# Kernel optimization log

Measured on AMD Instinct MI355X. Metric: run time of the kernel, lower is better.

## Reference

```python
import jax, jax.numpy as jnp
import numpy as np

EPS = 1e-4  # clamp floor used by RecFunction
B, C, D = 8192, 62, 8


def _rec(M):
    # Rectify SPD matrix: clamp eigenvalues at EPS. For SPD input, torch.svd's
    # (U, S) coincide with the eigendecomposition, so eigh is the faithful
    # (and efficient, symmetry-exploiting) batched equivalent.
    w, U = jnp.linalg.eigh(M)                      # w: [B,D], U: [B,D,D]
    return (U * jnp.maximum(w, EPS)[..., None, :]) @ jnp.swapaxes(U, -1, -2)


def _logm(M):
    # Matrix log via eigendecomposition (eigenvalues >= EPS after _rec).
    w, U = jnp.linalg.eigh(M)
    return (U * jnp.log(w)[..., None, :]) @ jnp.swapaxes(U, -1, -2)


def setup_inputs() -> dict:
    key = jax.random.key(0)
    kx, k1, k2, k3 = jax.random.split(key, 4)
    A = jax.random.normal(kx, (B, C, C), dtype=jnp.float32)
    X = (A @ jnp.swapaxes(A, 1, 2)) / C            # SPD covariance-like input [B,62,62]
    w1 = jax.random.normal(k1, (C, D), dtype=jnp.float32)
    w2 = jax.random.normal(k2, (D, D), dtype=jnp.float32)
    fc = jax.random.normal(k3, (D * D, 2), dtype=jnp.float32)
    return {"X": X, "w1": w1, "w2": w2, "fc": fc}


def reference(X, w1, w2, fc):
    # BiMap 62->8, rectify
    out = _rec(jnp.einsum('ca,bcd,de->bae', w1, X, w1))   # [B,8,8]
    # BiMap 8->8, rectify
    out = _rec(jnp.einsum('ca,bcd,de->bae', w2, out, w2)) # [B,8,8]
    # LogEig
    out = _logm(out)                                      # [B,8,8]
    feat = out.reshape(out.shape[0], -1)                  # [B,64]
    logits = feat @ fc                                    # [B,2]
    return jax.nn.log_softmax(logits, axis=1), feat
```

## Files before the change

kernel.cpp:

```cpp
#include <hip/hip_runtime.h>
#include <math.h>

#define B_TOTAL 8192
#define C_DIM 62
#define CC (C_DIM * C_DIM)
#define EPSV 1e-4f
#define NSWEEP 4
#define WSTRIDE 72
#define YSTR 9


template<int M> __device__ __forceinline__ float sx(float x) {
  int xi = __builtin_bit_cast(int, x);
  int r;
  if constexpr (M == 1)      r = __builtin_amdgcn_update_dpp(xi, xi, 0xB1, 0xF, 0xF, false);
  else if constexpr (M == 2) r = __builtin_amdgcn_update_dpp(xi, xi, 0x4E, 0xF, 0xF, false);
  else if constexpr (M == 3) r = __builtin_amdgcn_update_dpp(xi, xi, 0x1B, 0xF, 0xF, false);
  else                       r = __builtin_amdgcn_ds_swizzle(xi, (M << 10) | 0x1F);
  return __builtin_bit_cast(float, r);
}

__device__ __forceinline__ void xperm8(float r[8], const int e) {
  const bool b0 = (e & 1) != 0, b1 = (e & 2) != 0, b2 = (e & 4) != 0;
  float t0[8], t1[8];
#pragma unroll
  for (int j = 0; j < 8; ++j) t0[j] = b0 ? r[j ^ 1] : r[j];
#pragma unroll
  for (int j = 0; j < 8; ++j) t1[j] = b1 ? t0[j ^ 2] : t0[j];
#pragma unroll
  for (int j = 0; j < 8; ++j) r[j] = b2 ? t1[j ^ 4] : t1[j];
}

template<int M>
__device__ __forceinline__ void jstage(float ar[8], float pr[8], const int e) {
  constexpr int HB = (M >= 4) ? 4 : ((M >= 2) ? 2 : 1);
  constexpr int A1 = (M == 1) ? 2 : 1;
  constexpr int A2 = (M <= 3) ? 4 : 2;
  const bool low = (e & HB) == 0;
  float d_oth = sx<M>(ar[0]);
  float o_oth = sx<M>(ar[M]);
  float apq = 0.5f * (ar[M] + o_oth);
  float app = low ? ar[0] : d_oth;
  float aqq = low ? d_oth : ar[0];
  float taun = aqq - app;
  float den = fabsf(taun) + sqrtf(fmaf(taun, taun, 4.f * apq * apq)) + 1e-38f;
  float t = (2.f * apq) * copysignf(1.f, taun) * __builtin_amdgcn_rcpf(den);
  float c = rsqrtf(fmaf(t, t, 1.f));
  float s = t * c;
  float cg[8], sg[8];
  cg[0] = c;  sg[0] = s;
  cg[A1] = sx<A1>(c);  sg[A1] = sx<A1>(s);
  cg[A2] = sx<A2>(c);  sg[A2] = sx<A2>(s);
  cg[A1 ^ A2] = sx<A2>(cg[A1]);  sg[A1 ^ A2] = sx<A2>(sg[A1]);
  float an[8], pn[8];
#pragma unroll
  for (int d = 0; d < 8; ++d) {
    constexpr int T0 = 0;
    const int rep = (d == T0 || d == A1 || d == A2 || d == (A1 ^ A2)) ? d : (d ^ M);
    const bool flip = (d & HB) != 0;
    float sD = sg[rep];
    float ss = (low != flip) ? -sD : sD;
    an[d] = fmaf(cg[rep], ar[d], ss * ar[d ^ M]);
    pn[d] = fmaf(cg[rep], pr[d], ss * pr[d ^ M]);
  }
#pragma unroll
  for (int d = 0; d < 8; ++d) pr[d] = pn[d];
  float scol = low ? -s : s;
  float aoth[8];
#pragma unroll
  for (int d = 0; d < 8; ++d) aoth[d] = sx<M>(an[d ^ M]);
#pragma unroll
  for (int d = 0; d < 8; ++d) ar[d] = fmaf(c, an[d], scol * aoth[d]);
}

__device__ __forceinline__ void jacobi8rel(float ar[8], float u[8], const int e) {
  float pr[8];
#pragma unroll
  for (int i = 0; i < 8; ++i) pr[i] = (i == 0) ? 1.f : 0.f;
#pragma unroll 1
  for (int sweep = 0; sweep < NSWEEP; ++sweep) {
    jstage<1>(ar, pr, e);
    jstage<2>(ar, pr, e);
    jstage<3>(ar, pr, e);
    jstage<4>(ar, pr, e);
    jstage<5>(ar, pr, e);
    jstage<6>(ar, pr, e);
    jstage<7>(ar, pr, e);
  }
  u[0] = pr[0];
  u[1] = sx<1>(pr[1]);
  u[2] = sx<2>(pr[2]);
  u[3] = sx<3>(pr[3]);
  u[4] = sx<4>(pr[4]);
  u[5] = sx<5>(pr[5]);
  u[6] = sx<6>(pr[6]);
  u[7] = sx<7>(pr[7]);
  xperm8(u, e);
}

__global__ __launch_bounds__(64) void spdnet_kernel(
    const float* __restrict__ X, const float* __restrict__ w1,
    const float* __restrict__ w2, const float* __restrict__ fc,
    float* __restrict__ out) {
  __shared__ __align__(16) float w1s[C_DIM * 8];
  __shared__ float Ys[C_DIM * YSTR];
  __shared__ float M1s[8 * 64];
  __shared__ __align__(16) float Wbuf[8 * WSTRIDE];
  __shared__ float lwbuf[64];
  __shared__ float w2s[64];
  __shared__ float fcs[128];
  const int lane = threadIdx.x;
  const int b0 = blockIdx.x * 8;

  w2s[lane] = w2[lane];
  fcs[lane] = fc[lane];
  fcs[lane + 64] = fc[lane + 64];
  if (lane < C_DIM) {
    *(float4*)(w1s + lane * 8)     = *(const float4*)(w1 + lane * 8);
    *(float4*)(w1s + lane * 8 + 4) = *(const float4*)(w1 + lane * 8 + 4);
  }

  float xrA[C_DIM], xrB[C_DIM];
  if (lane < C_DIM) {
    const float* row = X + (size_t)b0 * CC + lane * C_DIM;
#pragma unroll
    for (int k = 0; k < 31; ++k) {
      float2 t = *(const float2*)(row + 2 * k);
      xrA[2 * k] = t.x; xrA[2 * k + 1] = t.y;
    }
  }
  __syncthreads();

  auto loadrow = [&](float* r, int g) {
    if (lane < C_DIM) {
      const float* row = X + (size_t)(b0 + g) * CC + lane * C_DIM;
#pragma unroll
      for (int k = 0; k < 31; ++k) {
        float2 t = *(const float2*)(row + 2 * k);
        r[2 * k] = t.x; r[2 * k + 1] = t.y;
      }
    }
  };
  auto computeA = [&](const float* xr, int g) {
    if (lane < C_DIM) {
      float a0=0.f,a1=0.f,a2=0.f,a3=0.f,a4=0.f,a5=0.f,a6=0.f,a7=0.f;
#pragma unroll
      for (int d = 0; d < C_DIM; ++d) {
        float x = xr[d];
        const float* wr = w1 + d * 8;
        a0 = fmaf(x, wr[0], a0); a1 = fmaf(x, wr[1], a1);
        a2 = fmaf(x, wr[2], a2); a3 = fmaf(x, wr[3], a3);
        a4 = fmaf(x, wr[4], a4); a5 = fmaf(x, wr[5], a5);
        a6 = fmaf(x, wr[6], a6); a7 = fmaf(x, wr[7], a7);
      }
      float* yr = Ys + lane * YSTR;
      yr[0]=a0; yr[1]=a1; yr[2]=a2; yr[3]=a3;
      yr[4]=a4; yr[5]=a5; yr[6]=a6; yr[7]=a7;
    }
    __syncthreads();
    {
      const int a_ = lane >> 3, e_ = lane & 7;
      float s = 0.f;
#pragma unroll
      for (int c = 0; c < C_DIM; ++c)
        s = fmaf(w1s[c * 8 + a_], Ys[c * YSTR + e_], s);
      M1s[g * 64 + lane] = s;
    }
    __syncthreads();
  };

#pragma unroll 1
  for (int g = 0; g < 8; g += 2) {
    loadrow(xrB, g + 1);
    computeA(xrA, g);
    if (g + 2 < 8) loadrow(xrA, g + 2);
    computeA(xrB, g + 1);
  }

  const int e = lane & 7;
  const int g = lane >> 3;
  float a[8], u[8], m2[8];
  float* Wg = &Wbuf[g * WSTRIDE];

#pragma unroll
  for (int j = 0; j < 8; ++j) a[j] = M1s[g * 64 + e * 8 + j];

  {
    float t[8];
#pragma unroll
    for (int j = 0; j < 8; ++j) t[j] = 0.f;
#pragma unroll
    for (int k = 0; k < 8; ++k) {
      float4 q0 = *(const float4*)(w2s + k * 8);
      float4 q1 = *(const float4*)(w2s + k * 8 + 4);
      t[0] = fmaf(a[k], q0.x, t[0]); t[1] = fmaf(a[k], q0.y, t[1]);
      t[2] = fmaf(a[k], q0.z, t[2]); t[3] = fmaf(a[k], q0.w, t[3]);
      t[4] = fmaf(a[k], q1.x, t[4]); t[5] = fmaf(a[k], q1.y, t[5]);
      t[6] = fmaf(a[k], q1.z, t[6]); t[7] = fmaf(a[k], q1.w, t[7]);
    }
#pragma unroll
    for (int j = 0; j < 8; ++j) Wg[e * 8 + j] = t[j];
  }
  __syncthreads();
  {
    float tcol[8];
#pragma unroll
    for (int k = 0; k < 8; ++k) tcol[k] = Wg[k * 8 + e];
#pragma unroll
    for (int i = 0; i < 8; ++i) m2[i] = 0.f;
#pragma unroll
    for (int k = 0; k < 8; ++k) {
      float4 q0 = *(const float4*)(w2s + k * 8);
      float4 q1 = *(const float4*)(w2s + k * 8 + 4);
      m2[0] = fmaf(q0.x, tcol[k], m2[0]); m2[1] = fmaf(q0.y, tcol[k], m2[1]);
      m2[2] = fmaf(q0.z, tcol[k], m2[2]); m2[3] = fmaf(q0.w, tcol[k], m2[3]);
      m2[4] = fmaf(q1.x, tcol[k], m2[4]); m2[5] = fmaf(q1.y, tcol[k], m2[5]);
      m2[6] = fmaf(q1.z, tcol[k], m2[6]); m2[7] = fmaf(q1.w, tcol[k], m2[7]);
    }
  }
  __syncthreads();

  xperm8(m2, e);
  jacobi8rel(m2, u, e);
  float lw = logf(fmaxf(m2[0], EPSV));
#pragma unroll
  for (int i = 0; i < 8; ++i) Wg[e * 8 + i] = u[i];
  lwbuf[g * 8 + e] = lw;
  __syncthreads();
  {
    float mk[8];
#pragma unroll
    for (int k = 0; k < 8; ++k) mk[k] = lwbuf[g * 8 + k] * Wg[k * 8 + e];
    float fcol[8];
#pragma unroll
    for (int i = 0; i < 8; ++i) fcol[i] = 0.f;
#pragma unroll
    for (int k = 0; k < 8; ++k) {
      float4 q0 = *(const float4*)&Wg[k * 8 + 0];
      float4 q1 = *(const float4*)&Wg[k * 8 + 4];
      fcol[0] = fmaf(q0.x, mk[k], fcol[0]); fcol[1] = fmaf(q0.y, mk[k], fcol[1]);
      fcol[2] = fmaf(q0.z, mk[k], fcol[2]); fcol[3] = fmaf(q0.w, mk[k], fcol[3]);
      fcol[4] = fmaf(q1.x, mk[k], fcol[4]); fcol[5] = fmaf(q1.y, mk[k], fcol[5]);
      fcol[6] = fmaf(q1.z, mk[k], fcol[6]); fcol[7] = fmaf(q1.w, mk[k], fcol[7]);
    }
    float l0 = 0.f, l1 = 0.f;
    const int b = b0 + g;
    float* featg = out + 2 * (size_t)B_TOTAL + (size_t)b * 64;
#pragma unroll
    for (int i = 0; i < 8; ++i) {
      featg[i * 8 + e] = fcol[i];
      l0 = fmaf(fcol[i], fcs[(i * 8 + e) * 2 + 0], l0);
      l1 = fmaf(fcol[i], fcs[(i * 8 + e) * 2 + 1], l1);
    }
    l0 += sx<1>(l0); l0 += sx<2>(l0); l0 += sx<4>(l0);
    l1 += sx<1>(l1); l1 += sx<2>(l1); l1 += sx<4>(l1);
    float mx = fmaxf(l0, l1);
    float lse = mx + logf(expf(l0 - mx) + expf(l1 - mx));
    if (e < 2) out[(size_t)b * 2 + e] = (e ? l1 : l0) - lse;
  }
}

extern "C" void kernel_launch(void* const* d_in, const int* in_sizes, int n_in,
                              void* d_out, int out_size, void* d_ws, size_t ws_size,
                              hipStream_t stream) {
  const float* X  = (const float*)d_in[0];
  const float* w1 = (const float*)d_in[1];
  const float* w2 = (const float*)d_in[2];
  const float* fc = (const float*)d_in[3];
  float* out = (float*)d_out;

  spdnet_kernel<<<B_TOTAL / 8, 64, 0, stream>>>(X, w1, w2, fc, out);
}
```

Measured before the change: 37.69 us.

## Process 16 batches per block with two waves, interleave two Jacobi solves in one wave

Blocks now handle 16 matrices with 128 threads: both wavefronts load and project their own 8 X matrices through the 62->8 BiMap. After that, only wave 0 runs the second BiMap, the Jacobi eigensolver and the LogEig/FC tail, interleaving two independent 8x8 solves per lane to expose instruction-level parallelism. This halves the grid and amortizes weight loads, but wave 1 idles through the serial Jacobi phase, and register pressure grows from holding two matrices per lane.

```diff
diff --git a/kernel.cpp b/kernel.cpp
--- a/kernel.cpp
+++ b/kernel.cpp
@@ -6,9 +6,9 @@
 #define CC (C_DIM * C_DIM)
 #define EPSV 1e-4f
 #define NSWEEP 4
+#define NBB 16
 #define WSTRIDE 72
 #define YSTR 9
-
 
 template<int M> __device__ __forceinline__ float sx(float x) {
   int xi = __builtin_bit_cast(int, x);
@@ -32,97 +32,118 @@
 }
 
 template<int M>
-__device__ __forceinline__ void jstage(float ar[8], float pr[8], const int e) {
+__device__ __forceinline__ void jstage2(float ar1[8], float pr1[8],
+                                        float ar2[8], float pr2[8], const int e) {
   constexpr int HB = (M >= 4) ? 4 : ((M >= 2) ? 2 : 1);
   constexpr int A1 = (M == 1) ? 2 : 1;
   constexpr int A2 = (M <= 3) ? 4 : 2;
   const bool low = (e & HB) == 0;
-  float d_oth = sx<M>(ar[0]);
-  float o_oth = sx<M>(ar[M]);
-  float apq = 0.5f * (ar[M] + o_oth);
-  float app = low ? ar[0] : d_oth;
-  float aqq = low ? d_oth : ar[0];
-  float taun = aqq - app;
-  float den = fabsf(taun) + sqrtf(fmaf(taun, taun, 4.f * apq * apq)) + 1e-38f;
-  float t = (2.f * apq) * copysignf(1.f, taun) * __builtin_amdgcn_rcpf(den);
-  float c = rsqrtf(fmaf(t, t, 1.f));
-  float s = t * c;
-  float cg[8], sg[8];
-  cg[0] = c;  sg[0] = s;
-  cg[A1] = sx<A1>(c);  sg[A1] = sx<A1>(s);
-  cg[A2] = sx<A2>(c);  sg[A2] = sx<A2>(s);
-  cg[A1 ^ A2] = sx<A2>(cg[A1]);  sg[A1 ^ A2] = sx<A2>(sg[A1]);
-  float an[8], pn[8];
+  float d1 = sx<M>(ar1[0]);
+  float d2 = sx<M>(ar2[0]);
+  float o1 = sx<M>(ar1[M]);
+  float o2 = sx<M>(ar2[M]);
+  float apq1 = 0.5f * (ar1[M] + o1);
+  float apq2 = 0.5f * (ar2[M] + o2);
+  float app1 = low ? ar1[0] : d1, aqq1 = low ? d1 : ar1[0];
+  float app2 = low ? ar2[0] : d2, aqq2 = low ? d2 : ar2[0];
+  float tn1 = aqq1 - app1;
+  float tn2 = aqq2 - app2;
+  float den1 = fabsf(tn1) + sqrtf(fmaf(tn1, tn1, 4.f * apq1 * apq1)) + 1e-38f;
+  float den2 = fabsf(tn2) + sqrtf(fmaf(tn2, tn2, 4.f * apq2 * apq2)) + 1e-38f;
+  float t1 = (2.f * apq1) * copysignf(1.f, tn1) * __builtin_amdgcn_rcpf(den1);
+  float t2 = (2.f * apq2) * copysignf(1.f, tn2) * __builtin_amdgcn_rcpf(den2);
+  float c1 = rsqrtf(fmaf(t1, t1, 1.f));
+  float c2 = rsqrtf(fmaf(t2, t2, 1.f));
+  float s1 = t1 * c1;
+  float s2 = t2 * c2;
+  float cg1[8], sg1[8], cg2[8], sg2[8];
+  cg1[0] = c1; sg1[0] = s1; cg2[0] = c2; sg2[0] = s2;
+  cg1[A1] = sx<A1>(c1); cg2[A1] = sx<A1>(c2);
+  sg1[A1] = sx<A1>(s1); sg2[A1] = sx<A1>(s2);
+  cg1[A2] = sx<A2>(c1); cg2[A2] = sx<A2>(c2);
+  sg1[A2] = sx<A2>(s1); sg2[A2] = sx<A2>(s2);
+  cg1[A1 ^ A2] = sx<A2>(cg1[A1]); cg2[A1 ^ A2] = sx<A2>(cg2[A1]);
+  sg1[A1 ^ A2] = sx<A2>(sg1[A1]); sg2[A1 ^ A2] = sx<A2>(sg2[A1]);
+  float an1[8], pn1[8], an2[8], pn2[8];
 #pragma unroll
   for (int d = 0; d < 8; ++d) {
-    constexpr int T0 = 0;
-    const int rep = (d == T0 || d == A1 || d == A2 || d == (A1 ^ A2)) ? d : (d ^ M);
+    const int rep = (d == 0 || d == A1 || d == A2 || d == (A1 ^ A2)) ? d : (d ^ M);
     const bool flip = (d & HB) != 0;
-    float sD = sg[rep];
-    float ss = (low != flip) ? -sD : sD;
-    an[d] = fmaf(cg[rep], ar[d], ss * ar[d ^ M]);
-    pn[d] = fmaf(cg[rep], pr[d], ss * pr[d ^ M]);
-  }
-#pragma unroll
-  for (int d = 0; d < 8; ++d) pr[d] = pn[d];
-  float scol = low ? -s : s;
-  float aoth[8];
-#pragma unroll
-  for (int d = 0; d < 8; ++d) aoth[d] = sx<M>(an[d ^ M]);
-#pragma unroll
-  for (int d = 0; d < 8; ++d) ar[d] = fmaf(c, an[d], scol * aoth[d]);
-}
-
-__device__ __forceinline__ void jacobi8rel(float ar[8], float u[8], const int e) {
-  float pr[8];
-#pragma unroll
-  for (int i = 0; i < 8; ++i) pr[i] = (i == 0) ? 1.f : 0.f;
+    float ss1 = (low != flip) ? -sg1[rep] : sg1[rep];
+    float ss2 = (low != flip) ? -sg2[rep] : sg2[rep];
+    an1[d] = fmaf(cg1[rep], ar1[d], ss1 * ar1[d ^ M]);
+    an2[d] = fmaf(cg2[rep], ar2[d], ss2 * ar2[d ^ M]);
+    pn1[d] = fmaf(cg1[rep], pr1[d], ss1 * pr1[d ^ M]);
+    pn2[d] = fmaf(cg2[rep], pr2[d], ss2 * pr2[d ^ M]);
+  }
+#pragma unroll
+  for (int d = 0; d < 8; ++d) { pr1[d] = pn1[d]; pr2[d] = pn2[d]; }
+  float sc1 = low ? -s1 : s1;
+  float sc2 = low ? -s2 : s2;
+  float ao1[8], ao2[8];
+#pragma unroll
+  for (int d = 0; d < 8; ++d) { ao1[d] = sx<M>(an1[d ^ M]); ao2[d] = sx<M>(an2[d ^ M]); }
+#pragma unroll
+  for (int d = 0; d < 8; ++d) {
+    ar1[d] = fmaf(c1, an1[d], sc1 * ao1[d]);
+    ar2[d] = fmaf(c2, an2[d], sc2 * ao2[d]);
+  }
+}
+
+__device__ __forceinline__ void jacobi8rel2(float ar1[8], float u1[8],
+                                            float ar2[8], float u2[8], const int e) {
+  float pr1[8], pr2[8];
+#pragma unroll
+  for (int i = 0; i < 8; ++i) { pr1[i] = (i == 0) ? 1.f : 0.f; pr2[i] = pr1[i]; }
 #pragma unroll 1
   for (int sweep = 0; sweep < NSWEEP; ++sweep) {
-    jstage<1>(ar, pr, e);
-    jstage<2>(ar, pr, e);
-    jstage<3>(ar, pr, e);
-    jstage<4>(ar, pr, e);
-    jstage<5>(ar, pr, e);
-    jstage<6>(ar, pr, e);
-    jstage<7>(ar, pr, e);
-  }
-  u[0] = pr[0];
-  u[1] = sx<1>(pr[1]);
-  u[2] = sx<2>(pr[2]);
-  u[3] = sx<3>(pr[3]);
-  u[4] = sx<4>(pr[4]);
-  u[5] = sx<5>(pr[5]);
-  u[6] = sx<6>(pr[6]);
-  u[7] = sx<7>(pr[7]);
-  xperm8(u, e);
-}
-
-__global__ __launch_bounds__(64) void spdnet_kernel(
+    jstage2<1>(ar1, pr1, ar2, pr2, e);
+    jstage2<2>(ar1, pr1, ar2, pr2, e);
+    jstage2<3>(ar1, pr1, ar2, pr2, e);
+    jstage2<4>(ar1, pr1, ar2, pr2, e);
+    jstage2<5>(ar1, pr1, ar2, pr2, e);
+    jstage2<6>(ar1, pr1, ar2, pr2, e);
+    jstage2<7>(ar1, pr1, ar2, pr2, e);
+  }
+  u1[0] = pr1[0];                u2[0] = pr2[0];
+  u1[1] = sx<1>(pr1[1]);         u2[1] = sx<1>(pr2[1]);
+  u1[2] = sx<2>(pr1[2]);         u2[2] = sx<2>(pr2[2]);
+  u1[3] = sx<3>(pr1[3]);         u2[3] = sx<3>(pr2[3]);
+  u1[4] = sx<4>(pr1[4]);         u2[4] = sx<4>(pr2[4]);
+  u1[5] = sx<5>(pr1[5]);         u2[5] = sx<5>(pr2[5]);
+  u1[6] = sx<6>(pr1[6]);         u2[6] = sx<6>(pr2[6]);
+  u1[7] = sx<7>(pr1[7]);         u2[7] = sx<7>(pr2[7]);
+  xperm8(u1, e);
+  xperm8(u2, e);
+}
+
+__global__ __launch_bounds__(128) void spdnet_kernel(
     const float* __restrict__ X, const float* __restrict__ w1,
     const float* __restrict__ w2, const float* __restrict__ fc,
     float* __restrict__ out) {
   __shared__ __align__(16) float w1s[C_DIM * 8];
-  __shared__ float Ys[C_DIM * YSTR];
-  __shared__ float M1s[8 * 64];
-  __shared__ __align__(16) float Wbuf[8 * WSTRIDE];
-  __shared__ float lwbuf[64];
+  __shared__ float Ys[2][C_DIM * YSTR];
+  __shared__ float M1s[NBB * 64];
+  __shared__ __align__(16) float Wbuf[NBB * WSTRIDE];
+  __shared__ float lwbuf[NBB * 8];
   __shared__ float w2s[64];
   __shared__ float fcs[128];
-  const int lane = threadIdx.x;
-  const int b0 = blockIdx.x * 8;
-
-  w2s[lane] = w2[lane];
-  fcs[lane] = fc[lane];
-  fcs[lane + 64] = fc[lane + 64];
-  if (lane < C_DIM) {
-    *(float4*)(w1s + lane * 8)     = *(const float4*)(w1 + lane * 8);
-    *(float4*)(w1s + lane * 8 + 4) = *(const float4*)(w1 + lane * 8 + 4);
+  const int tid = threadIdx.x;
+  const int lane = tid & 63;
+  const int wv = tid >> 6;
+  const int b0 = blockIdx.x * NBB;
+  const int b0w = b0 + wv * 8;
+
+  if (tid < 64) w2s[tid] = w2[tid];
+  fcs[tid] = fc[tid];
+  if (tid < C_DIM) {
+    *(float4*)(w1s + tid * 8)     = *(const float4*)(w1 + tid * 8);
+    *(float4*)(w1s + tid * 8 + 4) = *(const float4*)(w1 + tid * 8 + 4);
   }
 
   float xrA[C_DIM], xrB[C_DIM];
   if (lane < C_DIM) {
-    const float* row = X + (size_t)b0 * CC + lane * C_DIM;
+    const float* row = X + (size_t)b0w * CC + lane * C_DIM;
 #pragma unroll
     for (int k = 0; k < 31; ++k) {
       float2 t = *(const float2*)(row + 2 * k);
@@ -133,7 +154,7 @@
 
   auto loadrow = [&](float* r, int g) {
     if (lane < C_DIM) {
-      const float* row = X + (size_t)(b0 + g) * CC + lane * C_DIM;
+      const float* row = X + (size_t)(b0w + g) * CC + lane * C_DIM;
 #pragma unroll
       for (int k = 0; k < 31; ++k) {
         float2 t = *(const float2*)(row + 2 * k);
@@ -153,7 +174,7 @@
         a4 = fmaf(x, wr[4], a4); a5 = fmaf(x, wr[5], a5);
         a6 = fmaf(x, wr[6], a6); a7 = fmaf(x, wr[7], a7);
       }
-      float* yr = Ys + lane * YSTR;
+      float* yr = Ys[wv] + lane * YSTR;
       yr[0]=a0; yr[1]=a1; yr[2]=a2; yr[3]=a3;
       yr[4]=a4; yr[5]=a5; yr[6]=a6; yr[7]=a7;
     }
@@ -163,8 +184,8 @@
       float s = 0.f;
 #pragma unroll
       for (int c = 0; c < C_DIM; ++c)
-        s = fmaf(w1s[c * 8 + a_], Ys[c * YSTR + e_], s);
-      M1s[g * 64 + lane] = s;
+        s = fmaf(w1s[c * 8 + a_], Ys[wv][c * YSTR + e_], s);
+      M1s[(wv * 8 + g) * 64 + lane] = s;
     }
     __syncthreads();
   };
@@ -178,85 +199,120 @@
   }
 
   const int e = lane & 7;
-  const int g = lane >> 3;
-  float a[8], u[8], m2[8];
-  float* Wg = &Wbuf[g * WSTRIDE];
-
-#pragma unroll
-  for (int j = 0; j < 8; ++j) a[j] = M1s[g * 64 + e * 8 + j];
-
-  {
-    float t[8];
-#pragma unroll
-    for (int j = 0; j < 8; ++j) t[j] = 0.f;
+  const int gg = lane >> 3;
+  float a1r[8], a2r[8], u1[8], u2[8], m21[8], m22[8];
+  float* Wg1 = &Wbuf[gg * WSTRIDE];
+  float* Wg2 = &Wbuf[(gg + 8) * WSTRIDE];
+
+  if (wv == 0) {
+#pragma unroll
+    for (int j = 0; j < 8; ++j) {
+      a1r[j] = M1s[gg * 64 + e * 8 + j];
+      a2r[j] = M1s[(gg + 8) * 64 + e * 8 + j];
+    }
+    float t1[8], t2[8];
+#pragma unroll
+    for (int j = 0; j < 8; ++j) { t1[j] = 0.f; t2[j] = 0.f; }
 #pragma unroll
     for (int k = 0; k < 8; ++k) {
       float4 q0 = *(const float4*)(w2s + k * 8);
       float4 q1 = *(const float4*)(w2s + k * 8 + 4);
-      t[0] = fmaf(a[k], q0.x, t[0]); t[1] = fmaf(a[k], q0.y, t[1]);
-      t[2] = fmaf(a[k], q0.z, t[2]); t[3] = fmaf(a[k], q0.w, t[3]);
-      t[4] = fmaf(a[k], q1.x, t[4]); t[5] = fmaf(a[k], q1.y, t[5]);
-      t[6] = fmaf(a[k], q1.z, t[6]); t[7] = fmaf(a[k], q1.w, t[7]);
-    }
-#pragma unroll
-    for (int j = 0; j < 8; ++j) Wg[e * 8 + j] = t[j];
+      t1[0] = fmaf(a1r[k], q0.x, t1[0]); t2[0] = fmaf(a2r[k], q0.x, t2[0]);
+      t1[1] = fmaf(a1r[k], q0.y, t1[1]); t2[1] = fmaf(a2r[k], q0.y, t2[1]);
+      t1[2] = fmaf(a1r[k], q0.z, t1[2]); t2[2] = fmaf(a2r[k], q0.z, t2[2]);
+      t1[3] = fmaf(a1r[k], q0.w, t1[3]); t2[3] = fmaf(a2r[k], q0.w, t2[3]);
+      t1[4] = fmaf(a1r[k], q1.x, t1[4]); t2[4] = fmaf(a2r[k], q1.x, t2[4]);
+      t1[5] = fmaf(a1r[k], q1.y, t1[5]); t2[5] = fmaf(a2r[k], q1.y, t2[5]);
+      t1[6] = fmaf(a1r[k], q1.z, t1[6]); t2[6] = fmaf(a2r[k], q1.z, t2[6]);
+      t1[7] = fmaf(a1r[k], q1.w, t1[7]); t2[7] = fmaf(a2r[k], q1.w, t2[7]);
+    }
+#pragma unroll
+    for (int j = 0; j < 8; ++j) { Wg1[e * 8 + j] = t1[j]; Wg2[e * 8 + j] = t2[j]; }
   }
   __syncthreads();
-  {
-    float tcol[8];
-#pragma unroll
-    for (int k = 0; k < 8; ++k) tcol[k] = Wg[k * 8 + e];
-#pragma unroll
-    for (int i = 0; i < 8; ++i) m2[i] = 0.f;
+  if (wv == 0) {
+    float tc1[8], tc2[8];
+#pragma unroll
+    for (int k = 0; k < 8; ++k) { tc1[k] = Wg1[k * 8 + e]; tc2[k] = Wg2[k * 8 + e]; }
+#pragma unroll
+    for (int i = 0; i < 8; ++i) { m21[i] = 0.f; m22[i] = 0.f; }
 #pragma unroll
     for (int k = 0; k < 8; ++k) {
       float4 q0 = *(const float4*)(w2s + k * 8);
       float4 q1 = *(const float4*)(w2s + k * 8 + 4);
-      m2[0] = fmaf(q0.x, tcol[k], m2[0]); m2[1] = fmaf(q0.y, tcol[k], m2[1]);
-      m2[2] = fmaf(q0.z, tcol[k], m2[2]); m2[3] = fmaf(q0.w, tcol[k], m2[3]);
-      m2[4] = fmaf(q1.x, tcol[k], m2[4]); m2[5] = fmaf(q1.y, tcol[k], m2[5]);
-      m2[6] = fmaf(q1.z, tcol[k], m2[6]); m2[7] = fmaf(q1.w, tcol[k], m2[7]);
+      m21[0] = fmaf(q0.x, tc1[k], m21[0]); m22[0] = fmaf(q0.x, tc2[k], m22[0]);
+      m21[1] = fmaf(q0.y, tc1[k], m21[1]); m22[1] = fmaf(q0.y, tc2[k], m22[1]);
+      m21[2] = fmaf(q0.z, tc1[k], m21[2]); m22[2] = fmaf(q0.z, tc2[k], m22[2]);
+      m21[3] = fmaf(q0.w, tc1[k], m21[3]); m22[3] = fmaf(q0.w, tc2[k], m22[3]);
+      m21[4] = fmaf(q1.x, tc1[k], m21[4]); m22[4] = fmaf(q1.x, tc2[k], m22[4]);
+      m21[5] = fmaf(q1.y, tc1[k], m21[5]); m22[5] = fmaf(q1.y, tc2[k], m22[5]);
+      m21[6] = fmaf(q1.z, tc1[k], m21[6]); m22[6] = fmaf(q1.z, tc2[k], m22[6]);
+      m21[7] = fmaf(q1.w, tc1[k], m21[7]); m22[7] = fmaf(q1.w, tc2[k], m22[7]);
     }
   }
   __syncthreads();
-
-  xperm8(m2, e);
-  jacobi8rel(m2, u, e);
-  float lw = logf(fmaxf(m2[0], EPSV));
-#pragma unroll
-  for (int i = 0; i < 8; ++i) Wg[e * 8 + i] = u[i];
-  lwbuf[g * 8 + e] = lw;
+  if (wv == 0) {
+    xperm8(m21, e);
+    xperm8(m22, e);
+    jacobi8rel2(m21, u1, m22, u2, e);
+    float lw1 = logf(fmaxf(m21[0], EPSV));
+    float lw2 = logf(fmaxf(m22[0], EPSV));
+#pragma unroll
+    for (int i = 0; i < 8; ++i) { Wg1[e * 8 + i] = u1[i]; Wg2[e * 8 + i] = u2[i]; }
+    lwbuf[gg * 8 + e] = lw1;
+    lwbuf[(gg + 8) * 8 + e] = lw2;
+  }
   __syncthreads();
-  {
-    float mk[8];
-#pragma unroll
-    for (int k = 0; k < 8; ++k) mk[k] = lwbuf[g * 8 + k] * Wg[k * 8 + e];
-    float fcol[8];
-#pragma unroll
-    for (int i = 0; i < 8; ++i) fcol[i] = 0.f;
+  if (wv == 0) {
+    float mk1[8], mk2[8];
 #pragma unroll
     for (int k = 0; k < 8; ++k) {
-      float4 q0 = *(const float4*)&Wg[k * 8 + 0];
-      float4 q1 = *(const float4*)&Wg[k * 8 + 4];
-      fcol[0] = fmaf(q0.x, mk[k], fcol[0]); fcol[1] = fmaf(q0.y, mk[k], fcol[1]);
-      fcol[2] = fmaf(q0.z, mk[k], fcol[2]); fcol[3] = fmaf(q0.w, mk[k], fcol[3]);
-      fcol[4] = fmaf(q1.x, mk[k], fcol[4]); fcol[5] = fmaf(q1.y, mk[k], fcol[5]);
-      fcol[6] = fmaf(q1.z, mk[k], fcol[6]); fcol[7] = fmaf(q1.w, mk[k], fcol[7]);
-    }
-    float l0 = 0.f, l1 = 0.f;
-    const int b = b0 + g;
-    float* featg = out + 2 * (size_t)B_TOTAL + (size_t)b * 64;
+      mk1[k] = lwbuf[gg * 8 + k] * Wg1[k * 8 + e];
+      mk2[k] = lwbuf[(gg + 8) * 8 + k] * Wg2[k * 8 + e];
+    }
+    float f1[8], f2[8];
+#pragma unroll
+    for (int i = 0; i < 8; ++i) { f1[i] = 0.f; f2[i] = 0.f; }
+#pragma unroll
+    for (int k = 0; k < 8; ++k) {
+      float4 q0 = *(const float4*)&Wg1[k * 8 + 0];
+      float4 q1 = *(const float4*)&Wg1[k * 8 + 4];
+      float4 r0 = *(const float4*)&Wg2[k * 8 + 0];
+      float4 r1 = *(const float4*)&Wg2[k * 8 + 4];
+      f1[0] = fmaf(q0.x, mk1[k], f1[0]); f2[0] = fmaf(r0.x, mk2[k], f2[0]);
+      f1[1] = fmaf(q0.y, mk1[k], f1[1]); f2[1] = fmaf(r0.y, mk2[k], f2[1]);
+      f1[2] = fmaf(q0.z, mk1[k], f1[2]); f2[2] = fmaf(r0.z, mk2[k], f2[2]);
+      f1[3] = fmaf(q0.w, mk1[k], f1[3]); f2[3] = fmaf(r0.w, mk2[k], f2[3]);
+      f1[4] = fmaf(q1.x, mk1[k], f1[4]); f2[4] = fmaf(r1.x, mk2[k], f2[4]);
+      f1[5] = fmaf(q1.y, mk1[k], f1[5]); f2[5] = fmaf(r1.y, mk2[k], f2[5]);
+      f1[6] = fmaf(q1.z, mk1[k], f1[6]); f2[6] = fmaf(r1.z, mk2[k], f2[6]);
+      f1[7] = fmaf(q1.w, mk1[k], f1[7]); f2[7] = fmaf(r1.w, mk2[k], f2[7]);
+    }
+    float l01 = 0.f, l11 = 0.f, l02 = 0.f, l12 = 0.f;
+    const int b1 = b0 + gg, b2 = b0 + gg + 8;
+    float* fg1 = out + 2 * (size_t)B_TOTAL + (size_t)b1 * 64;
+    float* fg2 = out + 2 * (size_t)B_TOTAL + (size_t)b2 * 64;
 #pragma unroll
     for (int i = 0; i < 8; ++i) {
-      featg[i * 8 + e] = fcol[i];
-      l0 = fmaf(fcol[i], fcs[(i * 8 + e) * 2 + 0], l0);
-      l1 = fmaf(fcol[i], fcs[(i * 8 + e) * 2 + 1], l1);
-    }
-    l0 += sx<1>(l0); l0 += sx<2>(l0); l0 += sx<4>(l0);
-    l1 += sx<1>(l1); l1 += sx<2>(l1); l1 += sx<4>(l1);
-    float mx = fmaxf(l0, l1);
-    float lse = mx + logf(expf(l0 - mx) + expf(l1 - mx));
-    if (e < 2) out[(size_t)b * 2 + e] = (e ? l1 : l0) - lse;
+      fg1[i * 8 + e] = f1[i];
+      fg2[i * 8 + e] = f2[i];
+      l01 = fmaf(f1[i], fcs[(i * 8 + e) * 2 + 0], l01);
+      l11 = fmaf(f1[i], fcs[(i * 8 + e) * 2 + 1], l11);
+      l02 = fmaf(f2[i], fcs[(i * 8 + e) * 2 + 0], l02);
+      l12 = fmaf(f2[i], fcs[(i * 8 + e) * 2 + 1], l12);
+    }
+    l01 += sx<1>(l01); l01 += sx<2>(l01); l01 += sx<4>(l01);
+    l11 += sx<1>(l11); l11 += sx<2>(l11); l11 += sx<4>(l11);
+    l02 += sx<1>(l02); l02 += sx<2>(l02); l02 += sx<4>(l02);
+    l12 += sx<1>(l12); l12 += sx<2>(l12); l12 += sx<4>(l12);
+    float mx1 = fmaxf(l01, l11);
+    float ls1 = mx1 + logf(expf(l01 - mx1) + expf(l11 - mx1));
+    float mx2 = fmaxf(l02, l12);
+    float ls2 = mx2 + logf(expf(l02 - mx2) + expf(l12 - mx2));
+    if (e < 2) {
+      out[(size_t)b1 * 2 + e] = (e ? l11 : l01) - ls1;
+      out[(size_t)b2 * 2 + e] = (e ? l12 : l02) - ls2;
+    }
   }
 }
 
@@ -269,5 +325,5 @@
   const float* fc = (const float*)d_in[3];
   float* out = (float*)d_out;
 
-  spdnet_kernel<<<B_TOTAL / 8, 64, 0, stream>>>(X, w1, w2, fc, out);
-}
+  spdnet_kernel<<<B_TOTAL / NBB, 128, 0, stream>>>(X, w1, w2, fc, out);
+}
```

New measurement: 47.09 us. 1.25x slower.

## Split first BiMap stage across two waves per block

Applied to the files above, without the earlier changes.

Block size grows from 64 to 128 threads. Each wave handles 4 of the block's 8 matrices in the memory-heavy 62x62 projection stage, using its own Ys buffer, so the X loads and FMAs for that stage are split across two waves. The later 8x8 eigen stages still run on only the first wave while the second wave idles at barriers. The gain should come from more parallelism in the bandwidth-bound load phase, at the cost of more registers per block and idle threads in the tail.

```diff
diff --git a/kernel.cpp b/kernel.cpp
--- a/kernel.cpp
+++ b/kernel.cpp
@@ -55,8 +55,7 @@
   float an[8], pn[8];
 #pragma unroll
   for (int d = 0; d < 8; ++d) {
-    constexpr int T0 = 0;
-    const int rep = (d == T0 || d == A1 || d == A2 || d == (A1 ^ A2)) ? d : (d ^ M);
+    const int rep = (d == 0 || d == A1 || d == A2 || d == (A1 ^ A2)) ? d : (d ^ M);
     const bool flip = (d & HB) != 0;
     float sD = sg[rep];
     float ss = (low != flip) ? -sD : sD;
@@ -98,31 +97,33 @@
   xperm8(u, e);
 }
 
-__global__ __launch_bounds__(64) void spdnet_kernel(
+__global__ __launch_bounds__(128) void spdnet_kernel(
     const float* __restrict__ X, const float* __restrict__ w1,
     const float* __restrict__ w2, const float* __restrict__ fc,
     float* __restrict__ out) {
   __shared__ __align__(16) float w1s[C_DIM * 8];
-  __shared__ float Ys[C_DIM * YSTR];
+  __shared__ float Ys[2][C_DIM * YSTR];
   __shared__ float M1s[8 * 64];
   __shared__ __align__(16) float Wbuf[8 * WSTRIDE];
   __shared__ float lwbuf[64];
   __shared__ float w2s[64];
   __shared__ float fcs[128];
-  const int lane = threadIdx.x;
+  const int tid = threadIdx.x;
+  const int lane = tid & 63;
+  const int wv = tid >> 6;
   const int b0 = blockIdx.x * 8;
-
-  w2s[lane] = w2[lane];
-  fcs[lane] = fc[lane];
-  fcs[lane + 64] = fc[lane + 64];
-  if (lane < C_DIM) {
-    *(float4*)(w1s + lane * 8)     = *(const float4*)(w1 + lane * 8);
-    *(float4*)(w1s + lane * 8 + 4) = *(const float4*)(w1 + lane * 8 + 4);
+  const int b0w = b0 + wv * 4;
+
+  if (tid < 64) w2s[tid] = w2[tid];
+  fcs[tid] = fc[tid];
+  if (tid < C_DIM) {
+    *(float4*)(w1s + tid * 8)     = *(const float4*)(w1 + tid * 8);
+    *(float4*)(w1s + tid * 8 + 4) = *(const float4*)(w1 + tid * 8 + 4);
   }
 
   float xrA[C_DIM], xrB[C_DIM];
   if (lane < C_DIM) {
-    const float* row = X + (size_t)b0 * CC + lane * C_DIM;
+    const float* row = X + (size_t)b0w * CC + lane * C_DIM;
 #pragma unroll
     for (int k = 0; k < 31; ++k) {
       float2 t = *(const float2*)(row + 2 * k);
@@ -133,7 +134,7 @@
 
   auto loadrow = [&](float* r, int g) {
     if (lane < C_DIM) {
-      const float* row = X + (size_t)(b0 + g) * CC + lane * C_DIM;
+      const float* row = X + (size_t)(b0w + g) * CC + lane * C_DIM;
 #pragma unroll
       for (int k = 0; k < 31; ++k) {
         float2 t = *(const float2*)(row + 2 * k);
@@ -153,7 +154,7 @@
         a4 = fmaf(x, wr[4], a4); a5 = fmaf(x, wr[5], a5);
         a6 = fmaf(x, wr[6], a6); a7 = fmaf(x, wr[7], a7);
       }
-      float* yr = Ys + lane * YSTR;
+      float* yr = Ys[wv] + lane * YSTR;
       yr[0]=a0; yr[1]=a1; yr[2]=a2; yr[3]=a3;
       yr[4]=a4; yr[5]=a5; yr[6]=a6; yr[7]=a7;
     }
@@ -163,29 +164,29 @@
       float s = 0.f;
 #pragma unroll
       for (int c = 0; c < C_DIM; ++c)
-        s = fmaf(w1s[c * 8 + a_], Ys[c * YSTR + e_], s);
-      M1s[g * 64 + lane] = s;
+        s = fmaf(w1s[c * 8 + a_], Ys[wv][c * YSTR + e_], s);
+      M1s[(wv * 4 + g) * 64 + lane] = s;
     }
     __syncthreads();
   };
 
 #pragma unroll 1
-  for (int g = 0; g < 8; g += 2) {
+  for (int g = 0; g < 4; g += 2) {
     loadrow(xrB, g + 1);
     computeA(xrA, g);
-    if (g + 2 < 8) loadrow(xrA, g + 2);
+    if (g + 2 < 4) loadrow(xrA, g + 2);
     computeA(xrB, g + 1);
   }
 
-  const int e = lane & 7;
-  const int g = lane >> 3;
+  const int e = tid & 7;
+  const int g = (tid >> 3) & 7;
+  const bool bact = (tid < 64);
   float a[8], u[8], m2[8];
   float* Wg = &Wbuf[g * WSTRIDE];
 
-#pragma unroll
-  for (int j = 0; j < 8; ++j) a[j] = M1s[g * 64 + e * 8 + j];
-
-  {
+  if (bact) {
+#pragma unroll
+    for (int j = 0; j < 8; ++j) a[j] = M1s[g * 64 + e * 8 + j];
     float t[8];
 #pragma unroll
     for (int j = 0; j < 8; ++j) t[j] = 0.f;
@@ -202,7 +203,7 @@
     for (int j = 0; j < 8; ++j) Wg[e * 8 + j] = t[j];
   }
   __syncthreads();
-  {
+  if (bact) {
     float tcol[8];
 #pragma unroll
     for (int k = 0; k < 8; ++k) tcol[k] = Wg[k * 8 + e];
@@ -219,15 +220,16 @@
     }
   }
   __syncthreads();
-
-  xperm8(m2, e);
-  jacobi8rel(m2, u, e);
-  float lw = logf(fmaxf(m2[0], EPSV));
-#pragma unroll
-  for (int i = 0; i < 8; ++i) Wg[e * 8 + i] = u[i];
-  lwbuf[g * 8 + e] = lw;
-  __syncthreads();
-  {
+  if (bact) {
+    xperm8(m2, e);
+    jacobi8rel(m2, u, e);
+    float lw = logf(fmaxf(m2[0], EPSV));
+#pragma unroll
+    for (int i = 0; i < 8; ++i) Wg[e * 8 + i] = u[i];
+    lwbuf[g * 8 + e] = lw;
+  }
+  __syncthreads();
+  if (bact) {
     float mk[8];
 #pragma unroll
     for (int k = 0; k < 8; ++k) mk[k] = lwbuf[g * 8 + k] * Wg[k * 8 + e];
@@ -269,5 +271,5 @@
   const float* fc = (const float*)d_in[3];
   float* out = (float*)d_out;
 
-  spdnet_kernel<<<B_TOTAL / 8, 64, 0, stream>>>(X, w1, w2, fc, out);
-}
+  spdnet_kernel<<<B_TOTAL / 8, 128, 0, stream>>>(X, w1, w2, fc, out);
+}
```

Measured after the change: 39.92 us. 1.06x slower.
